# Kernel tuning notes

Measured on AMD Instinct MI355X. Metric: run time of the kernel, lower is better.

Reference implementation:

```python
import jax, jax.numpy as jnp
import numpy as np

D_MODEL = 2048
N_EXPERTS = 64
TOP_K = 8
N_TOKENS = 16384


def setup_inputs() -> dict:
    key = jax.random.key(0)
    k1, k2 = jax.random.split(key)
    x_flat = jax.random.normal(k1, (N_TOKENS, D_MODEL), dtype=jnp.float32)
    # nn.Linear(d_model, n_experts) weight has shape [n_experts, d_model]
    gate_w = jax.random.normal(k2, (N_EXPERTS, D_MODEL), dtype=jnp.float32) * (1.0 / np.sqrt(D_MODEL))
    return {"x_flat": x_flat, "gate_w": gate_w}


def reference(x_flat, gate_w):
    # logits = x_flat @ gate_w.T : [tokens, n_experts]
    logits = jnp.einsum("td,ed->te", x_flat, gate_w)
    full_probs = jax.nn.softmax(logits, axis=-1)
    topk_logits, topk_idx = jax.lax.top_k(logits, TOP_K)
    topk_weights = jax.nn.softmax(topk_logits, axis=-1)
    return topk_idx, topk_weights, full_probs, logits
```

## Files before the change

### kernel.cpp

```cpp
#include <hip/hip_runtime.h>
#include <math.h>

#define D_MODEL   2048
#define N_EXPERTS 64
#define TOP_K     8
#define N_TOKENS  16384
#define TOK_TILE  64
#define NTHREADS  512
#define WS_NEED   (64*4*3*64*16)

typedef __attribute__((ext_vector_type(8))) short bf16x8;
typedef __attribute__((ext_vector_type(4))) float f32x4;
typedef __attribute__((ext_vector_type(4))) int   i32x4;

union FragU { i32x4 i; bf16x8 h; };

__device__ __forceinline__ void split3(float x, unsigned &h, unsigned &m, unsigned &l) {
    unsigned ux = __float_as_uint(x);
    h = ux & 0xffff0000u;
    float mf = x - __uint_as_float(h);
    unsigned um = __float_as_uint(mf) & 0xffff0000u;
    float lf = mf - __uint_as_float(um);
    m = um;
    l = __float_as_uint(lf) & 0xffff0000u;
}

__global__ __launch_bounds__(256) void pack_w_kernel(const float* __restrict__ gw,
                                                     unsigned* __restrict__ wp) {
    const int g    = blockIdx.x * 256 + threadIdx.x;
    const int d    = g & 3;
    const int lane = (g >> 2) & 63;
    const int rest = g >> 8;
    const int v    = rest % 3;
    const int t    = rest / 3;
    const int fr   = t & 3;
    const int ks   = t >> 2;
    const int e    = fr * 16 + (lane & 15);
    const int k    = ks * 32 + (lane >> 4) * 8 + 2 * d;
    const float w0 = gw[(size_t)e * D_MODEL + k];
    const float w1 = gw[(size_t)e * D_MODEL + k + 1];
    unsigned h0, m0, l0, h1, m1, l1;
    split3(w0, h0, m0, l0);
    split3(w1, h1, m1, l1);
    const unsigned c0 = (v == 0) ? h0 : ((v == 1) ? m0 : l0);
    const unsigned c1 = (v == 0) ? h1 : ((v == 1) ? m1 : l1);
    wp[g] = (c0 >> 16) | c1;
}

__device__ __forceinline__ void splitpack(const float4 a, const float4 b,
                                          FragU &ph, FragU &pm, FragU &pl) {
    const float f[8] = {a.x, a.y, a.z, a.w, b.x, b.y, b.z, b.w};
#pragma unroll
    for (int d = 0; d < 4; ++d) {
        unsigned h0, m0, l0, h1, m1, l1;
        split3(f[2 * d],     h0, m0, l0);
        split3(f[2 * d + 1], h1, m1, l1);
        ph.i[d] = (int)((h0 >> 16) | h1);
        pm.i[d] = (int)((m0 >> 16) | m1);
        pl.i[d] = (int)((l0 >> 16) | l1);
    }
}

#define MFMA(A_, B_, C_) C_ = __builtin_amdgcn_mfma_f32_16x16x32_bf16((A_).h, (B_).h, C_, 0, 0, 0)

__global__ __launch_bounds__(NTHREADS) void router_mfma(
    const float* __restrict__ x, const unsigned* __restrict__ wp,
    float* __restrict__ out)
{
    __shared__ __align__(16) float xs[2][TOK_TILE][64];
    __shared__ float lt[TOK_TILE][N_EXPERTS + 1];
    __shared__ float smax[TOK_TILE], srs[TOK_TILE];

    const int tid  = threadIdx.x;
    const int lane = tid & 63;
    const int wv   = tid >> 6;
    const int mrow = wv & 3;
    const int ncol = wv >> 2;
    const int m0   = blockIdx.x * TOK_TILE;

    const int lrow = lane & 15;
    const int lk   = lane >> 4;

    const int sr   = tid >> 3;
    const int s0   = tid & 7;
    const int wswz = (sr & 7) << 1;
    float* dstA = &xs[0][sr][4 * (s0 ^ wswz)];
    float* dstB = &xs[0][sr][4 * ((s0 ^ wswz) ^ 8)];
    const float* xsrc = x + (size_t)(m0 + sr) * D_MODEL + 4 * s0;

    float4 xa = *(const float4*)(xsrc);
    float4 xb = *(const float4*)(xsrc + 32);
    *(float4*)dstA = xa;
    *(float4*)dstB = xb;

    f32x4 acc0a = {0.f, 0.f, 0.f, 0.f};
    f32x4 acc0b = acc0a, acc1a = acc0a, acc1b = acc0a;

    const unsigned* wb = wp + (size_t)(ncol * 6) * 256 + lane * 4;
    const int arow = mrow * 16 + lrow;
    const int amsk = (lrow & 7) << 1;
    const int LBUF = TOK_TILE * 64;
    __syncthreads();

    for (int c = 0; c < 32; ++c) {
        if (c + 1 < 32) {
            xa = *(const float4*)(xsrc + (c + 1) * 64);
            xb = *(const float4*)(xsrc + (c + 1) * 64 + 32);
        }
        const float* xbuf = &xs[c & 1][0][0];
#pragma unroll
        for (int j = 0; j < 2; ++j) {
            const int ks = 2 * c + j;
            const unsigned* bt = wb + (size_t)ks * 3072;
            i32x4 B0h = *(const i32x4*)(bt +    0);
            i32x4 B0m = *(const i32x4*)(bt +  256);
            i32x4 B0l = *(const i32x4*)(bt +  512);
            i32x4 B1h = *(const i32x4*)(bt +  768);
            i32x4 B1m = *(const i32x4*)(bt + 1024);
            i32x4 B1l = *(const i32x4*)(bt + 1280);

            const int slot = (j * 8 + 2 * lk) ^ amsk;
            const float* ap = xbuf + arow * 64 + 4 * slot;
            const float4 Aa = *(const float4*)(ap);
            const float4 Ab = *(const float4*)(ap + 4);

            FragU ah, am, al;
            splitpack(Aa, Ab, ah, am, al);
            FragU b0h, b0m, b0l, b1h, b1m, b1l;
            b0h.i = B0h; b0m.i = B0m; b0l.i = B0l;
            b1h.i = B1h; b1m.i = B1m; b1l.i = B1l;

            MFMA(ah, b0h, acc0a); MFMA(am, b0h, acc0a); MFMA(al, b0h, acc0a);
            MFMA(ah, b0m, acc0b); MFMA(am, b0m, acc0b); MFMA(ah, b0l, acc0b);
            MFMA(ah, b1h, acc1a); MFMA(am, b1h, acc1a); MFMA(al, b1h, acc1a);
            MFMA(ah, b1m, acc1b); MFMA(am, b1m, acc1b); MFMA(ah, b1l, acc1b);
        }
        if (c + 1 < 32) {
            const int off = ((c + 1) & 1) * LBUF;
            *(float4*)(dstA + off) = xa;
            *(float4*)(dstB + off) = xb;
        }
        __syncthreads();
    }

#pragma unroll
    for (int r = 0; r < 4; ++r) {
        lt[mrow * 16 + lk * 4 + r][ncol * 32 +  0 + lrow] = acc0a[r] + acc0b[r];
        lt[mrow * 16 + lk * 4 + r][ncol * 32 + 16 + lrow] = acc1a[r] + acc1b[r];
    }
    __syncthreads();

    float* out_idx = out;
    float* out_w   = out + (size_t)N_TOKENS * TOP_K;
    float* out_p   = out + (size_t)2 * N_TOKENS * TOP_K;
    float* out_l   = out_p + (size_t)N_TOKENS * N_EXPERTS;

    if (tid < TOK_TILE) {
        const int t = tid;
        float tv[TOP_K];
        int   ti[TOP_K];
#pragma unroll
        for (int i = 0; i < TOP_K; ++i) { tv[i] = -INFINITY; ti[i] = 0; }
        float m = -INFINITY;

        for (int e = 0; e < N_EXPERTS; ++e) {
            const float v = lt[t][e];
            m = fmaxf(m, v);
            if (v > tv[TOP_K - 1]) {
#pragma unroll
                for (int j = TOP_K - 1; j >= 1; --j) {
                    const bool shift = (v > tv[j - 1]);
                    const bool here  = (v > tv[j]);
                    const float ntv = shift ? tv[j - 1] : (here ? v : tv[j]);
                    const int   nti = shift ? ti[j - 1] : (here ? e : ti[j]);
                    tv[j] = ntv; ti[j] = nti;
                }
                if (v > tv[0]) { tv[0] = v; ti[0] = e; }
            }
        }

        float s = 0.f;
        for (int e = 0; e < N_EXPERTS; ++e) s += expf(lt[t][e] - m);
        const float rs = 1.f / s;
        smax[t] = m;
        srs[t]  = rs;

        float ex[TOP_K];
        float wsum = 0.f;
#pragma unroll
        for (int i = 0; i < TOP_K; ++i) { ex[i] = expf(tv[i] - tv[0]); wsum += ex[i]; }
        const float rw = 1.f / wsum;

        const int tok = m0 + t;
#pragma unroll
        for (int i = 0; i < TOP_K; ++i) {
            out_idx[(size_t)tok * TOP_K + i] = (float)ti[i];
            out_w  [(size_t)tok * TOP_K + i] = ex[i] * rw;
        }
    }
    __syncthreads();

#pragma unroll
    for (int rep = 0; rep < 2; ++rep) {
        const int f = rep * (NTHREADS * 4) + tid * 4;
        const int t = f >> 6;
        const int e = f & 63;
        const float l0 = lt[t][e + 0];
        const float l1 = lt[t][e + 1];
        const float l2 = lt[t][e + 2];
        const float l3 = lt[t][e + 3];
        const float mm = smax[t];
        const float rr = srs[t];
        float4 pv = make_float4(expf(l0 - mm) * rr, expf(l1 - mm) * rr,
                                expf(l2 - mm) * rr, expf(l3 - mm) * rr);
        float4 lv = make_float4(l0, l1, l2, l3);
        const size_t gbase = (size_t)m0 * N_EXPERTS + f;
        *(float4*)(out_p + gbase) = pv;
        *(float4*)(out_l + gbase) = lv;
    }
}

__global__ __launch_bounds__(NTHREADS) void router_fallback(
    const float* __restrict__ x, const float* __restrict__ gw,
    float* __restrict__ out)
{
    __shared__ float xs[TOK_TILE][33];
    __shared__ float wsh[N_EXPERTS][36];
    __shared__ float lt[TOK_TILE][N_EXPERTS + 1];
    __shared__ float smax[TOK_TILE], srs[TOK_TILE];

    const int tid  = threadIdx.x;
    const int lane = tid & 63;
    const int wv   = tid >> 6;
    const int m0   = blockIdx.x * TOK_TILE;
    const int srow = tid >> 3;
    const int skq  = (tid & 7) * 4;

    const float* xsrc = x  + (size_t)(m0 + srow) * D_MODEL + skq;
    const float* wsrc = gw + (size_t)srow        * D_MODEL + skq;
    float4 xr = *(const float4*)(xsrc);
    float4 wr = *(const float4*)(wsrc);

    float acc[8];
#pragma unroll
    for (int i = 0; i < 8; ++i) acc[i] = 0.f;
    const int e0 = wv * 8;

    for (int c = 0; c < D_MODEL / 32; ++c) {
        xs[srow][skq] = xr.x; xs[srow][skq+1] = xr.y; xs[srow][skq+2] = xr.z; xs[srow][skq+3] = xr.w;
        *(float4*)&wsh[srow][skq] = wr;
        __syncthreads();
        if (c + 1 < D_MODEL / 32) {
            xr = *(const float4*)(xsrc + (c + 1) * 32);
            wr = *(const float4*)(wsrc + (c + 1) * 32);
        }
#pragma unroll 8
        for (int k4 = 0; k4 < 8; ++k4) {
            const float4 xv = *(const float4*)&xs[lane][k4 * 4];
#pragma unroll
            for (int e = 0; e < 8; ++e) {
                const float4 w4 = *(const float4*)&wsh[e0 + e][k4 * 4];
                acc[e] = fmaf(xv.x, w4.x, fmaf(xv.y, w4.y, fmaf(xv.z, w4.z, fmaf(xv.w, w4.w, acc[e]))));
            }
        }
        __syncthreads();
    }
#pragma unroll
    for (int e = 0; e < 8; ++e) lt[lane][e0 + e] = acc[e];
    __syncthreads();

    float* out_idx = out;
    float* out_w   = out + (size_t)N_TOKENS * TOP_K;
    float* out_p   = out + (size_t)2 * N_TOKENS * TOP_K;
    float* out_l   = out_p + (size_t)N_TOKENS * N_EXPERTS;

    if (tid < TOK_TILE) {
        const int t = tid;
        float tv[TOP_K]; int ti[TOP_K];
#pragma unroll
        for (int i = 0; i < TOP_K; ++i) { tv[i] = -INFINITY; ti[i] = 0; }
        float m = -INFINITY;
        for (int e = 0; e < N_EXPERTS; ++e) {
            const float v = lt[t][e];
            m = fmaxf(m, v);
            if (v > tv[TOP_K - 1]) {
#pragma unroll
                for (int j = TOP_K - 1; j >= 1; --j) {
                    const bool shift = (v > tv[j - 1]);
                    const bool here  = (v > tv[j]);
                    const float ntv = shift ? tv[j - 1] : (here ? v : tv[j]);
                    const int   nti = shift ? ti[j - 1] : (here ? e : ti[j]);
                    tv[j] = ntv; ti[j] = nti;
                }
                if (v > tv[0]) { tv[0] = v; ti[0] = e; }
            }
        }
        float s = 0.f;
        for (int e = 0; e < N_EXPERTS; ++e) s += expf(lt[t][e] - m);
        const float rs = 1.f / s;
        smax[t] = m; srs[t] = rs;
        float ex[TOP_K]; float wsum = 0.f;
#pragma unroll
        for (int i = 0; i < TOP_K; ++i) { ex[i] = expf(tv[i] - tv[0]); wsum += ex[i]; }
        const float rw = 1.f / wsum;
        const int tok = m0 + t;
#pragma unroll
        for (int i = 0; i < TOP_K; ++i) {
            out_idx[(size_t)tok * TOP_K + i] = (float)ti[i];
            out_w  [(size_t)tok * TOP_K + i] = ex[i] * rw;
        }
    }
    __syncthreads();
#pragma unroll
    for (int rep = 0; rep < 2; ++rep) {
        const int f = rep * (NTHREADS * 4) + tid * 4;
        const int t = f >> 6;
        const int e = f & 63;
        const float l0 = lt[t][e], l1 = lt[t][e+1], l2 = lt[t][e+2], l3 = lt[t][e+3];
        const float mm = smax[t], rr = srs[t];
        float4 pv = make_float4(expf(l0-mm)*rr, expf(l1-mm)*rr, expf(l2-mm)*rr, expf(l3-mm)*rr);
        float4 lv = make_float4(l0, l1, l2, l3);
        const size_t gbase = (size_t)m0 * N_EXPERTS + f;
        *(float4*)(out_p + gbase) = pv;
        *(float4*)(out_l + gbase) = lv;
    }
}

extern "C" void kernel_launch(void* const* d_in, const int* in_sizes, int n_in,
                              void* d_out, int out_size, void* d_ws, size_t ws_size,
                              hipStream_t stream) {
    const float* x  = (const float*)d_in[0];
    const float* gw = (const float*)d_in[1];
    float* out = (float*)d_out;
    if (ws_size >= (size_t)WS_NEED) {
        unsigned* wp = (unsigned*)d_ws;
        pack_w_kernel<<<dim3(WS_NEED / 4 / 256), dim3(256), 0, stream>>>(gw, wp);
        router_mfma<<<dim3(N_TOKENS / TOK_TILE), dim3(NTHREADS), 0, stream>>>(x, wp, out);
    } else {
        router_fallback<<<dim3(N_TOKENS / TOK_TILE), dim3(NTHREADS), 0, stream>>>(x, gw, out);
    }
}
```

Measured before the change: 74.20 us.

## Triple-buffer activation tiles with direct-to-LDS async loads and prefetch weight fragments

Replaces the register-staged double buffer for the x tile with a three-stage LDS ring filled by global_load_lds 16-byte async copies issued two chunks ahead. The swizzled layout is kept consistent between the copy destination and the MFMA reads. Packed weight fragments for the next chunk are now loaded into a second register set while the current chunk computes, hiding global latency of B. It also adds a min-blocks-per-CU hint of 2 to the launch bounds, which constrains register use and risks spills given the doubled B register arrays.

New measurement: 82.25 us. +10.8%, slower.

```diff
diff --git a/kernel.cpp b/kernel.cpp
--- a/kernel.cpp
+++ b/kernel.cpp
@@ -7,6 +7,7 @@
 #define N_TOKENS  16384
 #define TOK_TILE  64
 #define NTHREADS  512
+#define NCHUNK    32
 #define WS_NEED   (64*4*3*64*16)
 
 typedef __attribute__((ext_vector_type(8))) short bf16x8;
@@ -23,6 +24,12 @@
     float lf = mf - __uint_as_float(um);
     m = um;
     l = __float_as_uint(lf) & 0xffff0000u;
+}
+
+__device__ __forceinline__ void async_cp16(const float* g, float* l) {
+    __builtin_amdgcn_global_load_lds(
+        (const __attribute__((address_space(1))) void*)g,
+        (__attribute__((address_space(3))) void*)l, 16, 0, 0);
 }
 
 __global__ __launch_bounds__(256) void pack_w_kernel(const float* __restrict__ gw,
@@ -63,11 +70,11 @@
 
 #define MFMA(A_, B_, C_) C_ = __builtin_amdgcn_mfma_f32_16x16x32_bf16((A_).h, (B_).h, C_, 0, 0, 0)
 
-__global__ __launch_bounds__(NTHREADS) void router_mfma(
+__global__ __launch_bounds__(NTHREADS, 2) void router_mfma(
     const float* __restrict__ x, const unsigned* __restrict__ wp,
     float* __restrict__ out)
 {
-    __shared__ __align__(16) float xs[2][TOK_TILE][64];
+    __shared__ __align__(16) float xs[3][TOK_TILE][64];
     __shared__ float lt[TOK_TILE][N_EXPERTS + 1];
     __shared__ float smax[TOK_TILE], srs[TOK_TILE];
 
@@ -81,67 +88,95 @@
     const int lrow = lane & 15;
     const int lk   = lane >> 4;
 
-    const int sr   = tid >> 3;
-    const int s0   = tid & 7;
-    const int wswz = (sr & 7) << 1;
-    float* dstA = &xs[0][sr][4 * (s0 ^ wswz)];
-    float* dstB = &xs[0][sr][4 * ((s0 ^ wswz) ^ 8)];
-    const float* xsrc = x + (size_t)(m0 + sr) * D_MODEL + 4 * s0;
-
-    float4 xa = *(const float4*)(xsrc);
-    float4 xb = *(const float4*)(xsrc + 32);
-    *(float4*)dstA = xa;
-    *(float4*)dstB = xb;
+    float* xsflat = &xs[0][0][0];
+    const int LBUF = TOK_TILE * 64;
+
+    const int r0  = wv * 8 + (lane >> 4);
+    const int r1  = r0 + 4;
+    const float* src0 = x + (size_t)(m0 + r0) * D_MODEL + 4 * ((lane & 15) ^ (r0 & 7));
+    const float* src1 = x + (size_t)(m0 + r1) * D_MODEL + 4 * ((lane & 15) ^ (r1 & 7));
+    float* ldst = xsflat + wv * 512;
+
+    const int arow = mrow * 16 + lrow;
+    const int am   = lrow & 7;
+    const int offa0 = arow * 64 + 4 * (( 0 + 2 * lk)     ^ am);
+    const int offb0 = arow * 64 + 4 * (( 0 + 2 * lk + 1) ^ am);
+    const int offa1 = arow * 64 + 4 * (( 8 + 2 * lk)     ^ am);
+    const int offb1 = arow * 64 + 4 * (( 8 + 2 * lk + 1) ^ am);
+
+    const unsigned* wb = wp + (size_t)(ncol * 6) * 256 + lane * 4;
 
     f32x4 acc0a = {0.f, 0.f, 0.f, 0.f};
     f32x4 acc0b = acc0a, acc1a = acc0a, acc1b = acc0a;
 
-    const unsigned* wb = wp + (size_t)(ncol * 6) * 256 + lane * 4;
-    const int arow = mrow * 16 + lrow;
-    const int amsk = (lrow & 7) << 1;
-    const int LBUF = TOK_TILE * 64;
-    __syncthreads();
-
-    for (int c = 0; c < 32; ++c) {
-        if (c + 1 < 32) {
-            xa = *(const float4*)(xsrc + (c + 1) * 64);
-            xb = *(const float4*)(xsrc + (c + 1) * 64 + 32);
-        }
-        const float* xbuf = &xs[c & 1][0][0];
-#pragma unroll
-        for (int j = 0; j < 2; ++j) {
-            const int ks = 2 * c + j;
-            const unsigned* bt = wb + (size_t)ks * 3072;
-            i32x4 B0h = *(const i32x4*)(bt +    0);
-            i32x4 B0m = *(const i32x4*)(bt +  256);
-            i32x4 B0l = *(const i32x4*)(bt +  512);
-            i32x4 B1h = *(const i32x4*)(bt +  768);
-            i32x4 B1m = *(const i32x4*)(bt + 1024);
-            i32x4 B1l = *(const i32x4*)(bt + 1280);
-
-            const int slot = (j * 8 + 2 * lk) ^ amsk;
-            const float* ap = xbuf + arow * 64 + 4 * slot;
-            const float4 Aa = *(const float4*)(ap);
-            const float4 Ab = *(const float4*)(ap + 4);
-
-            FragU ah, am, al;
-            splitpack(Aa, Ab, ah, am, al);
-            FragU b0h, b0m, b0l, b1h, b1m, b1l;
-            b0h.i = B0h; b0m.i = B0m; b0l.i = B0l;
-            b1h.i = B1h; b1m.i = B1m; b1l.i = B1l;
-
-            MFMA(ah, b0h, acc0a); MFMA(am, b0h, acc0a); MFMA(al, b0h, acc0a);
-            MFMA(ah, b0m, acc0b); MFMA(am, b0m, acc0b); MFMA(ah, b0l, acc0b);
-            MFMA(ah, b1h, acc1a); MFMA(am, b1h, acc1a); MFMA(al, b1h, acc1a);
-            MFMA(ah, b1m, acc1b); MFMA(am, b1m, acc1b); MFMA(ah, b1l, acc1b);
-        }
-        if (c + 1 < 32) {
-            const int off = ((c + 1) & 1) * LBUF;
-            *(float4*)(dstA + off) = xa;
-            *(float4*)(dstB + off) = xb;
+    i32x4 BA[12], BB[12];
+
+#define STAGE_X(cN)                                                          \
+    if ((cN) < NCHUNK) {                                                     \
+        float* d_ = ldst + ((cN) % 3) * LBUF;                                \
+        async_cp16(src0 + (cN) * 64, d_);                                    \
+        async_cp16(src1 + (cN) * 64, d_ + 256);                              \
+    }
+
+#define LOAD_B(cN, Barr)                                                     \
+    if ((cN) < NCHUNK) {                                                     \
+        const unsigned* bt0_ = wb + (size_t)(2 * (cN)) * 3072;               \
+        const unsigned* bt1_ = bt0_ + 3072;                                  \
+        Barr[0]  = *(const i32x4*)(bt0_ +    0);                             \
+        Barr[1]  = *(const i32x4*)(bt0_ +  256);                             \
+        Barr[2]  = *(const i32x4*)(bt0_ +  512);                             \
+        Barr[3]  = *(const i32x4*)(bt0_ +  768);                             \
+        Barr[4]  = *(const i32x4*)(bt0_ + 1024);                             \
+        Barr[5]  = *(const i32x4*)(bt0_ + 1280);                             \
+        Barr[6]  = *(const i32x4*)(bt1_ +    0);                             \
+        Barr[7]  = *(const i32x4*)(bt1_ +  256);                             \
+        Barr[8]  = *(const i32x4*)(bt1_ +  512);                             \
+        Barr[9]  = *(const i32x4*)(bt1_ +  768);                             \
+        Barr[10] = *(const i32x4*)(bt1_ + 1024);                             \
+        Barr[11] = *(const i32x4*)(bt1_ + 1280);                             \
+    }
+
+#define COMPUTE(cN, Barr)                                                    \
+    {                                                                        \
+        const float* xb_ = xsflat + ((cN) % 3) * LBUF;                       \
+        _Pragma("unroll")                                                    \
+        for (int j = 0; j < 2; ++j) {                                        \
+            const float4 Aa = *(const float4*)(xb_ + (j ? offa1 : offa0));   \
+            const float4 Ab = *(const float4*)(xb_ + (j ? offb1 : offb0));   \
+            FragU ah, am_, al;                                               \
+            splitpack(Aa, Ab, ah, am_, al);                                  \
+            FragU b0h, b0m, b0l, b1h, b1m, b1l;                              \
+            b0h.i = Barr[j*6+0]; b0m.i = Barr[j*6+1]; b0l.i = Barr[j*6+2];   \
+            b1h.i = Barr[j*6+3]; b1m.i = Barr[j*6+4]; b1l.i = Barr[j*6+5];   \
+            MFMA(ah, b0h, acc0a); MFMA(am_, b0h, acc0a); MFMA(al, b0h, acc0a);\
+            MFMA(ah, b0m, acc0b); MFMA(am_, b0m, acc0b); MFMA(ah, b0l, acc0b);\
+            MFMA(ah, b1h, acc1a); MFMA(am_, b1h, acc1a); MFMA(al, b1h, acc1a);\
+            MFMA(ah, b1m, acc1b); MFMA(am_, b1m, acc1b); MFMA(ah, b1l, acc1b);\
+        }                                                                    \
+    }
+
+    STAGE_X(0);
+    STAGE_X(1);
+    LOAD_B(0, BA);
+    __syncthreads();
+
+#pragma unroll 2
+    for (int c = 0; c < NCHUNK; ++c) {
+        if (c & 1) {
+            STAGE_X(c + 2);
+            LOAD_B(c + 1, BA);
+            COMPUTE(c, BB);
+        } else {
+            STAGE_X(c + 2);
+            LOAD_B(c + 1, BB);
+            COMPUTE(c, BA);
         }
         __syncthreads();
     }
+
+#undef STAGE_X
+#undef LOAD_B
+#undef COMPUTE
 
 #pragma unroll
     for (int r = 0; r < 4; ++r) {
```

## Shrink token tile, add triple-buffered async global-to-LDS loads in router MFMA

Applied to the files above, without the earlier changes.

The MFMA router kernel now uses 16-token tiles with 256 threads (4 waves, each owning 16 experts), launching 1024 blocks instead of 256 and allowing 4 blocks per CU. The x staging changes from register round-trips into LDS to direct global_load_lds copies into a triple-buffered LDS ring, using raw s_barrier with manual vmcnt waits. This aims to raise occupancy and overlap memory with the split-bf16 MFMA work. The cost is that each block reloads the full packed weight set for only 16 tokens, which adds weight traffic. The hand-written waitcnt and barrier synchronisation also risks ordering bugs.

Result: slower. 83.24 us (+12.2%).

```diff
diff --git a/kernel.cpp b/kernel.cpp
--- a/kernel.cpp
+++ b/kernel.cpp
@@ -5,8 +5,9 @@
 #define N_EXPERTS 64
 #define TOP_K     8
 #define N_TOKENS  16384
-#define TOK_TILE  64
-#define NTHREADS  512
+#define TOK_TILE  16
+#define NTHREADS  256
+#define NCHUNK    32
 #define WS_NEED   (64*4*3*64*16)
 
 typedef __attribute__((ext_vector_type(8))) short bf16x8;
@@ -23,6 +24,12 @@
     float lf = mf - __uint_as_float(um);
     m = um;
     l = __float_as_uint(lf) & 0xffff0000u;
+}
+
+__device__ __forceinline__ void async_cp16(const float* g, float* l) {
+    __builtin_amdgcn_global_load_lds(
+        (const __attribute__((address_space(1))) void*)g,
+        (__attribute__((address_space(3))) void*)l, 16, 0, 0);
 }
 
 __global__ __launch_bounds__(256) void pack_w_kernel(const float* __restrict__ gw,
@@ -63,91 +70,89 @@
 
 #define MFMA(A_, B_, C_) C_ = __builtin_amdgcn_mfma_f32_16x16x32_bf16((A_).h, (B_).h, C_, 0, 0, 0)
 
-__global__ __launch_bounds__(NTHREADS) void router_mfma(
+#define CHUNK_BODY(c, bufi, DO_STAGE, sbuf)                                  \
+    {                                                                        \
+        const unsigned* bt0_ = wb + (size_t)(2 * (c)) * 3072;                \
+        const unsigned* bt1_ = bt0_ + 3072;                                  \
+        const i32x4 B0h = *(const i32x4*)(bt0_ +   0);                       \
+        const i32x4 B0m = *(const i32x4*)(bt0_ + 256);                       \
+        const i32x4 B0l = *(const i32x4*)(bt0_ + 512);                       \
+        const i32x4 B1h = *(const i32x4*)(bt1_ +   0);                       \
+        const i32x4 B1m = *(const i32x4*)(bt1_ + 256);                       \
+        const i32x4 B1l = *(const i32x4*)(bt1_ + 512);                       \
+        const float* xb_ = xsflat + (bufi) * LBUF;                           \
+        const float4 Aa0 = *(const float4*)(xb_ + offa0);                    \
+        const float4 Ab0 = *(const float4*)(xb_ + offb0);                    \
+        FragU ah, am_, al;                                                   \
+        splitpack(Aa0, Ab0, ah, am_, al);                                    \
+        FragU bh, bm, bl;                                                    \
+        bh.i = B0h; bm.i = B0m; bl.i = B0l;                                  \
+        MFMA(ah, bh, accA); MFMA(am_, bh, accA); MFMA(al, bh, accA);         \
+        MFMA(ah, bm, accB); MFMA(am_, bm, accB); MFMA(ah, bl, accB);         \
+        if (DO_STAGE)                                                        \
+            async_cp16(srcx + ((c) + 2) * 64, ldst + (sbuf) * LBUF);         \
+        const float4 Aa1 = *(const float4*)(xb_ + offa1);                    \
+        const float4 Ab1 = *(const float4*)(xb_ + offb1);                    \
+        splitpack(Aa1, Ab1, ah, am_, al);                                    \
+        bh.i = B1h; bm.i = B1m; bl.i = B1l;                                  \
+        MFMA(ah, bh, accA); MFMA(am_, bh, accA); MFMA(al, bh, accA);         \
+        MFMA(ah, bm, accB); MFMA(am_, bm, accB); MFMA(ah, bl, accB);         \
+        __builtin_amdgcn_s_barrier();                                        \
+    }
+
+__global__ __launch_bounds__(NTHREADS, 4) void router_mfma(
     const float* __restrict__ x, const unsigned* __restrict__ wp,
     float* __restrict__ out)
 {
-    __shared__ __align__(16) float xs[2][TOK_TILE][64];
+    __shared__ __align__(16) float xs[3][TOK_TILE][64];
     __shared__ float lt[TOK_TILE][N_EXPERTS + 1];
     __shared__ float smax[TOK_TILE], srs[TOK_TILE];
 
     const int tid  = threadIdx.x;
     const int lane = tid & 63;
     const int wv   = tid >> 6;
-    const int mrow = wv & 3;
-    const int ncol = wv >> 2;
     const int m0   = blockIdx.x * TOK_TILE;
 
     const int lrow = lane & 15;
     const int lk   = lane >> 4;
 
-    const int sr   = tid >> 3;
-    const int s0   = tid & 7;
-    const int wswz = (sr & 7) << 1;
-    float* dstA = &xs[0][sr][4 * (s0 ^ wswz)];
-    float* dstB = &xs[0][sr][4 * ((s0 ^ wswz) ^ 8)];
-    const float* xsrc = x + (size_t)(m0 + sr) * D_MODEL + 4 * s0;
-
-    float4 xa = *(const float4*)(xsrc);
-    float4 xb = *(const float4*)(xsrc + 32);
-    *(float4*)dstA = xa;
-    *(float4*)dstB = xb;
-
-    f32x4 acc0a = {0.f, 0.f, 0.f, 0.f};
-    f32x4 acc0b = acc0a, acc1a = acc0a, acc1b = acc0a;
-
-    const unsigned* wb = wp + (size_t)(ncol * 6) * 256 + lane * 4;
-    const int arow = mrow * 16 + lrow;
-    const int amsk = (lrow & 7) << 1;
+    float* xsflat = &xs[0][0][0];
     const int LBUF = TOK_TILE * 64;
-    __syncthreads();
-
-    for (int c = 0; c < 32; ++c) {
-        if (c + 1 < 32) {
-            xa = *(const float4*)(xsrc + (c + 1) * 64);
-            xb = *(const float4*)(xsrc + (c + 1) * 64 + 32);
-        }
-        const float* xbuf = &xs[c & 1][0][0];
-#pragma unroll
-        for (int j = 0; j < 2; ++j) {
-            const int ks = 2 * c + j;
-            const unsigned* bt = wb + (size_t)ks * 3072;
-            i32x4 B0h = *(const i32x4*)(bt +    0);
-            i32x4 B0m = *(const i32x4*)(bt +  256);
-            i32x4 B0l = *(const i32x4*)(bt +  512);
-            i32x4 B1h = *(const i32x4*)(bt +  768);
-            i32x4 B1m = *(const i32x4*)(bt + 1024);
-            i32x4 B1l = *(const i32x4*)(bt + 1280);
-
-            const int slot = (j * 8 + 2 * lk) ^ amsk;
-            const float* ap = xbuf + arow * 64 + 4 * slot;
-            const float4 Aa = *(const float4*)(ap);
-            const float4 Ab = *(const float4*)(ap + 4);
-
-            FragU ah, am, al;
-            splitpack(Aa, Ab, ah, am, al);
-            FragU b0h, b0m, b0l, b1h, b1m, b1l;
-            b0h.i = B0h; b0m.i = B0m; b0l.i = B0l;
-            b1h.i = B1h; b1m.i = B1m; b1l.i = B1l;
-
-            MFMA(ah, b0h, acc0a); MFMA(am, b0h, acc0a); MFMA(al, b0h, acc0a);
-            MFMA(ah, b0m, acc0b); MFMA(am, b0m, acc0b); MFMA(ah, b0l, acc0b);
-            MFMA(ah, b1h, acc1a); MFMA(am, b1h, acc1a); MFMA(al, b1h, acc1a);
-            MFMA(ah, b1m, acc1b); MFMA(am, b1m, acc1b); MFMA(ah, b1l, acc1b);
-        }
-        if (c + 1 < 32) {
-            const int off = ((c + 1) & 1) * LBUF;
-            *(float4*)(dstA + off) = xa;
-            *(float4*)(dstB + off) = xb;
-        }
-        __syncthreads();
-    }
-
-#pragma unroll
-    for (int r = 0; r < 4; ++r) {
-        lt[mrow * 16 + lk * 4 + r][ncol * 32 +  0 + lrow] = acc0a[r] + acc0b[r];
-        lt[mrow * 16 + lk * 4 + r][ncol * 32 + 16 + lrow] = acc1a[r] + acc1b[r];
-    }
+
+    const int rowx = wv * 4 + lk;
+    const float* srcx = x + (size_t)(m0 + rowx) * D_MODEL
+                        + 4 * ((lane & 15) ^ (rowx & 7));
+    float* ldst = xsflat + wv * 256;
+
+    const int am0  = lrow & 7;
+    const int offa0 = lrow * 64 + 4 * (( 2 * lk)     ^ am0);
+    const int offb0 = lrow * 64 + 4 * (( 2 * lk + 1) ^ am0);
+    const int offa1 = lrow * 64 + 4 * ((8 + 2 * lk)     ^ am0);
+    const int offb1 = lrow * 64 + 4 * ((8 + 2 * lk + 1) ^ am0);
+
+    const unsigned* wb = wp + (size_t)(wv * 3) * 256 + lane * 4;
+
+    f32x4 accA = {0.f, 0.f, 0.f, 0.f};
+    f32x4 accB = accA;
+
+    async_cp16(srcx,      ldst + 0 * LBUF);
+    async_cp16(srcx + 64, ldst + 1 * LBUF);
+    asm volatile("s_waitcnt vmcnt(1)" ::: "memory");
+    __builtin_amdgcn_s_barrier();
+
+    for (int cc = 0; cc < 30; cc += 3) {
+        CHUNK_BODY(cc + 0, 0, 1, 2);
+        CHUNK_BODY(cc + 1, 1, 1, 0);
+        CHUNK_BODY(cc + 2, 2, 1, 1);
+    }
+    CHUNK_BODY(30, 0, 0, 0);
+    CHUNK_BODY(31, 1, 0, 0);
+
+#undef CHUNK_BODY
+
+#pragma unroll
+    for (int r = 0; r < 4; ++r)
+        lt[lk * 4 + r][wv * 16 + lrow] = accA[r] + accB[r];
     __syncthreads();
 
     float* out_idx = out;
@@ -200,9 +205,8 @@
     }
     __syncthreads();
 
-#pragma unroll
-    for (int rep = 0; rep < 2; ++rep) {
-        const int f = rep * (NTHREADS * 4) + tid * 4;
+    {
+        const int f = tid * 4;
         const int t = f >> 6;
         const int e = f & 63;
         const float l0 = lt[t][e + 0];
@@ -220,19 +224,19 @@
     }
 }
 
-__global__ __launch_bounds__(NTHREADS) void router_fallback(
+__global__ __launch_bounds__(512) void router_fallback(
     const float* __restrict__ x, const float* __restrict__ gw,
     float* __restrict__ out)
 {
-    __shared__ float xs[TOK_TILE][33];
+    __shared__ float xs[64][33];
     __shared__ float wsh[N_EXPERTS][36];
-    __shared__ float lt[TOK_TILE][N_EXPERTS + 1];
-    __shared__ float smax[TOK_TILE], srs[TOK_TILE];
+    __shared__ float lt[64][N_EXPERTS + 1];
+    __shared__ float smax[64], srs[64];
 
     const int tid  = threadIdx.x;
     const int lane = tid & 63;
     const int wv   = tid >> 6;
-    const int m0   = blockIdx.x * TOK_TILE;
+    const int m0   = blockIdx.x * 64;
     const int srow = tid >> 3;
     const int skq  = (tid & 7) * 4;
 
@@ -274,7 +278,7 @@
     float* out_p   = out + (size_t)2 * N_TOKENS * TOP_K;
     float* out_l   = out_p + (size_t)N_TOKENS * N_EXPERTS;
 
-    if (tid < TOK_TILE) {
+    if (tid < 64) {
         const int t = tid;
         float tv[TOP_K]; int ti[TOP_K];
 #pragma unroll
@@ -313,7 +317,7 @@
     __syncthreads();
 #pragma unroll
     for (int rep = 0; rep < 2; ++rep) {
-        const int f = rep * (NTHREADS * 4) + tid * 4;
+        const int f = rep * (512 * 4) + tid * 4;
         const int t = f >> 6;
         const int e = f & 63;
         const float l0 = lt[t][e], l1 = lt[t][e+1], l2 = lt[t][e+2], l3 = lt[t][e+3];
@@ -337,6 +341,6 @@
         pack_w_kernel<<<dim3(WS_NEED / 4 / 256), dim3(256), 0, stream>>>(gw, wp);
         router_mfma<<<dim3(N_TOKENS / TOK_TILE), dim3(NTHREADS), 0, stream>>>(x, wp, out);
     } else {
-        router_fallback<<<dim3(N_TOKENS / TOK_TILE), dim3(NTHREADS), 0, stream>>>(x, gw, out);
-    }
-}
+        router_fallback<<<dim3(N_TOKENS / 64), dim3(512), 0, stream>>>(x, gw, out);
+    }
+}
```
